# Performance work log

Measured on AMD Instinct MI355X. Metric: run time of the kernel, lower is better.

## Reference

```python
import jax, jax.numpy as jnp
import numpy as np

P = 12           # AR order == number of rollout steps
N = 2048         # input_size (nodes)
B = 128          # batch
C = 1            # channels (only channel 0 used)


def setup_inputs() -> dict:
    key = jax.random.key(0)
    kx, kw = jax.random.split(key)
    x = jax.random.normal(kx, (B, N, C, P), dtype=jnp.float32)
    W = jax.random.normal(kw, (P, N, N), dtype=jnp.float32)
    return {"x": x, "W": W}


def reference(x, W):
    # x: [B, N, C, L]; take channel 0 and transpose -> [B, L(=p), N]
    xt = jnp.transpose(x[:, :, 0, :], (0, 2, 1))

    def step(xc, _):
        # einsum('ijk,bik->bij') followed by sum over i fuses to 'ijk,bik->bj'
        y = jnp.einsum('ijk,bik->bj', W, xc)              # [B, N]
        xc = jnp.concatenate([xc[:, 1:, :], y[:, None, :]], axis=1)  # shift window
        return xc, y

    _, ys = jax.lax.scan(step, xt, None, length=12)       # ys: [12, B, N]
    return jnp.transpose(ys, (1, 2, 0))                   # [B, N, 12]
```

## Files before the change

### kernel.cpp

```cpp
#include <hip/hip_runtime.h>
#include <stdint.h>


typedef _Float16 f16x8 __attribute__((ext_vector_type(8)));
typedef float    f32x4 __attribute__((ext_vector_type(4)));

#define B_ 128
#define N_ 2048
#define P_ 12
#define K_ (P_*N_)
#define NT 16
#define NKP (K_/64)

#define WPK_BYTES    ((size_t)NT*NKP*16384)
#define H_SLOT_BYTES ((size_t)B_*N_*2)
#define H_BYTES      (23*H_SLOT_BYTES)
#define CH_BYTES     ((size_t)B_*N_*2)
#define PF_BYTES     (78*CH_BYTES)
#define PFB_BYTES    (44*CH_BYTES)
#define WS_NEEDED    (WPK_BYTES + H_BYTES + PF_BYTES + PFB_BYTES)

__device__ __constant__ int E_TAB[11] = {7, 13, 18, 24, 29, 35, 40, 46, 51, 57, 62};

__device__ __forceinline__ float pow2f(int e) {
    return __uint_as_float((uint32_t)(127 + e) << 23);
}

union F16x8 { _Float16 h[8]; uint4 q; };
union F16x4v { _Float16 h[4]; uint2 q; };

__device__ __forceinline__ uint32_t h_off(int slot, int b, int k) {
    uint32_t t = (uint32_t)((b << 6) + ((k & 31) << 1)) ^ (uint32_t)((b & 7) << 4);
    return (uint32_t)slot * (uint32_t)H_SLOT_BYTES + (uint32_t)(k >> 5) * 8192u + t;
}
__device__ __forceinline__ size_t w_tile_base(int nt, int pk) {
    return ((size_t)nt * NKP + (size_t)pk) * 16384;
}

__global__ void prep_all(const float* __restrict__ x, const float* __restrict__ W,
                         char* __restrict__ Wp, char* __restrict__ H)
{
    __shared__ float tile[128][68];
    int bid = blockIdx.x, t = threadIdx.x;
    if (bid < 128) {
        int tg = bid * 256 + t;
        int b = tg >> 8;
        int n0 = (tg & 255) << 3;
        const float4* s4 = (const float4*)(x + ((size_t)b * N_ + n0) * P_);
        float4 tmp[24];
        #pragma unroll
        for (int i2 = 0; i2 < 24; ++i2) tmp[i2] = s4[i2];
        #pragma unroll
        for (int p = 0; p < 12; ++p) {
            F16x8 o;
            #pragma unroll
            for (int q = 0; q < 8; ++q) {
                int fi = q * 12 + p;
                float4 blk = tmp[fi >> 2];
                float f = ((fi & 3) == 0) ? blk.x : ((fi & 3) == 1) ? blk.y : ((fi & 3) == 2) ? blk.z : blk.w;
                o.h[q] = (_Float16)f;
            }
            *(uint4*)(H + h_off(p, b, n0)) = o.q;
        }
        return;
    }
    int u = bid - 128;
    int nt = u / NKP, pk = u % NKP;
    int i  = pk >> 5;
    int k0 = (pk & 31) << 6;
    int j0 = nt << 7;
    #pragma unroll
    for (int pass = 0; pass < 8; ++pass) {
        int jl = pass * 16 + (t >> 4);
        int kq = (t & 15) * 4;
        float4 v = *(const float4*)(W + ((size_t)i * N_ + (j0 + jl)) * N_ + k0 + kq);
        tile[jl][kq + 0] = v.x; tile[jl][kq + 1] = v.y;
        tile[jl][kq + 2] = v.z; tile[jl][kq + 3] = v.w;
    }
    __syncthreads();
    int ksub = t >> 7, c = t & 127;
    char* base = Wp + w_tile_base(nt, pk) + (ksub << 13);
    #pragma unroll
    for (int ko = 0; ko < 4; ++ko) {
        F16x8 o;
        #pragma unroll
        for (int q = 0; q < 8; ++q) o.h[q] = (_Float16)tile[c][ksub * 32 + ko * 8 + q];
        uint32_t off = (uint32_t)((c << 6) + (ko << 4)) ^ (uint32_t)((c & 7) << 4);
        *(uint4*)(base + off) = o.q;
    }
}

__device__ __forceinline__ void gemm_body(
        const char* __restrict__ Wp, const char* __restrict__ H,
        _Float16* __restrict__ part, char* ldsAB,
        int nt, int pk0, int slot, int k0, int nph)
{
    const int tid  = threadIdx.x;
    const int lane = tid & 63;
    const int wv   = tid >> 6;
    const int wr   = wv >> 1;
    const int wc   = wv & 1;
    const int l15  = lane & 15;
    const int ko   = lane >> 4;
    const int jbase = (nt << 7) + (wc << 6) + l15;

    uint32_t aoff[4], boff[4];
    #pragma unroll
    for (int m = 0; m < 4; ++m) {
        int row = (wr << 6) + (m << 4) + l15;
        aoff[m] = (uint32_t)((row << 6) + (ko << 4)) ^ (uint32_t)((row & 7) << 4);
    }
    #pragma unroll
    for (int nf = 0; nf < 4; ++nf) {
        int c = (wc << 6) + (nf << 4) + l15;
        boff[nf] = (uint32_t)((c << 6) + (ko << 4)) ^ (uint32_t)((c & 7) << 4);
    }

    auto stage = [&](int buf, int ph) {
        int k = k0 + (ph << 5);
        const char* sA = H + (size_t)slot * H_SLOT_BYTES + (uint32_t)((k >> 5) << 13);
        const char* sB = Wp + w_tile_base(nt, pk0 + (ph >> 1)) + (uint32_t)((ph & 1) << 13);
        #pragma unroll
        for (int j = 0; j < 2; ++j) {
            uint32_t o = (uint32_t)(j << 12) + (uint32_t)(tid << 4);
            uint32_t d = (uint32_t)(j << 12) + (uint32_t)(wv << 10);
            __builtin_amdgcn_global_load_lds(
                (const __attribute__((address_space(1))) void*)(sA + o),
                (__attribute__((address_space(3))) void*)(ldsAB + buf * 16384 + d), 16, 0, 0);
            __builtin_amdgcn_global_load_lds(
                (const __attribute__((address_space(1))) void*)(sB + o),
                (__attribute__((address_space(3))) void*)(ldsAB + buf * 16384 + 8192 + d), 16, 0, 0);
        }
    };

    f32x4 acc[4][4];
    #pragma unroll
    for (int m = 0; m < 4; ++m)
        #pragma unroll
        for (int n = 0; n < 4; ++n) acc[m][n] = (f32x4){0.f, 0.f, 0.f, 0.f};

    stage(0, 0);
    stage(1, 1);
    asm volatile("s_waitcnt vmcnt(4) lgkmcnt(0)" ::: "memory");
    __builtin_amdgcn_s_barrier();

    int cur = 0;
    #pragma unroll 1
    for (int ph = 0; ph < nph; ++ph) {
        int nxt2 = cur + 2; if (nxt2 >= 3) nxt2 -= 3;
        if (ph + 2 < nph) stage(nxt2, ph + 2);
        const char* lA = ldsAB + cur * 16384;
        const char* lB = lA + 8192;
        f16x8 ah[4], bf[4];
        #pragma unroll
        for (int m = 0; m < 4; ++m) ah[m] = *(const f16x8*)(lA + aoff[m]);
        #pragma unroll
        for (int nf = 0; nf < 4; ++nf) bf[nf] = *(const f16x8*)(lB + boff[nf]);
        #pragma unroll
        for (int m = 0; m < 4; ++m)
            #pragma unroll
            for (int nf = 0; nf < 4; ++nf)
                acc[m][nf] = __builtin_amdgcn_mfma_f32_16x16x32_f16(ah[m], bf[nf], acc[m][nf], 0, 0, 0);
        if (ph + 1 < nph) {
            if (ph + 2 < nph) asm volatile("s_waitcnt vmcnt(4) lgkmcnt(0)" ::: "memory");
            else              asm volatile("s_waitcnt vmcnt(0) lgkmcnt(0)" ::: "memory");
            __builtin_amdgcn_s_barrier();
        }
        ++cur; if (cur == 3) cur = 0;
    }

    const int r0 = (lane >> 4) << 2;
    _Float16* pb = part + ((size_t)((wr << 6) + r0)) * N_ + jbase;
    #pragma unroll
    for (int m = 0; m < 4; ++m)
        #pragma unroll
        for (int n = 0; n < 4; ++n)
            #pragma unroll
            for (int r = 0; r < 4; ++r)
                pb[(size_t)(m * 16 + r) * N_ + n * 16] = (_Float16)acc[m][n][r];
}

__global__ __launch_bounds__(256, 3) void gemm_F(
        const char* __restrict__ Wp, const char* __restrict__ H,
        _Float16* __restrict__ pF)
{
    __shared__ alignas(16) char ldsAB[3 * 16384];
    int bid = blockIdx.x;
    int bucket = bid / 96;
    int w = bid % 96;
    int m  = w >> 3;
    int g  = bucket * 8 + (w & 7);
    int j  = g >> 4;
    int nt = g & 15;
    int s  = j + m;
    if (s > 11) return;
    int t = m;
    int idx = t * 12 - t * (t - 1) / 2 + j;
    gemm_body(Wp, H, pF + (size_t)idx * (CH_BYTES / 2), ldsAB,
              nt, j * 32, s, 0, 64);
}

__global__ __launch_bounds__(256, 3) void gemm_FB(
        const char* __restrict__ Wp, const char* __restrict__ H,
        _Float16* __restrict__ pFB, int t)
{
    __shared__ alignas(16) char ldsAB[3 * 16384];
    int c = blockIdx.x >> 4, nt = blockIdx.x & 15;
    int j = c >> 2, sub = c & 3;
    int i = 12 - t + j;
    gemm_body(Wp, H, pFB + (size_t)c * (CH_BYTES / 2), ldsAB,
              nt, i * 32 + sub * 8, 12 + j, sub * 512, 16);
}

__global__ void reduce_step(const _Float16* __restrict__ pF, const _Float16* __restrict__ pFB,
                            float* __restrict__ out, char* __restrict__ H, int t)
{
    int tid = blockIdx.x * 256 + threadIdx.x;
    int b = tid >> 9;
    int n0 = (tid & 511) << 2;
    const size_t eo = (size_t)b * N_ + n0;
    float s0 = 0.f, s1 = 0.f, s2 = 0.f, s3 = 0.f;
    int baseT = t * 12 - t * (t - 1) / 2;
    int nF = 12 - t;
    #pragma unroll 4
    for (int f = 0; f < nF; ++f) {
        F16x4v p;
        p.q = *(const uint2*)(pF + (size_t)(baseT + f) * (CH_BYTES / 2) + eo);
        s0 += (float)p.h[0]; s1 += (float)p.h[1];
        s2 += (float)p.h[2]; s3 += (float)p.h[3];
    }
    #pragma unroll 4
    for (int c = 0; c < 4 * t; ++c) {
        float sc = pow2f(E_TAB[c >> 2]);
        F16x4v p;
        p.q = *(const uint2*)(pFB + (size_t)c * (CH_BYTES / 2) + eo);
        s0 += (float)p.h[0] * sc; s1 += (float)p.h[1] * sc;
        s2 += (float)p.h[2] * sc; s3 += (float)p.h[3] * sc;
    }
    float* ob = out + eo * P_ + t;
    ob[0 * P_] = s0; ob[1 * P_] = s1; ob[2 * P_] = s2; ob[3 * P_] = s3;
    if (t < 11) {
        float ds = pow2f(-E_TAB[t]);
        F16x4v o;
        o.h[0] = (_Float16)(s0 * ds); o.h[1] = (_Float16)(s1 * ds);
        o.h[2] = (_Float16)(s2 * ds); o.h[3] = (_Float16)(s3 * ds);
        *(uint2*)(H + h_off(12 + t, b, n0)) = o.q;
    }
}

__global__ void naive_step(const float* __restrict__ x, const float* __restrict__ W,
                           float* __restrict__ out, int t)
{
    int tid = blockIdx.x * 256 + threadIdx.x;
    int b = tid >> 11;
    int j = tid & (N_ - 1);
    float acc = 0.f;
    for (int i = 0; i < 12; ++i) {
        int g = t + i;
        const float* src = (g < 12) ? (x   + (size_t)b * (N_ * 12) + g)
                                    : (out + (size_t)b * (N_ * 12) + (g - 12));
        const float* wr = W + ((size_t)i * N_ + j) * N_;
        for (int k = 0; k < N_; ++k)
            acc += wr[k] * src[(size_t)k * 12];
    }
    out[((size_t)b * N_ + j) * 12 + t] = acc;
}

extern "C" void kernel_launch(void* const* d_in, const int* in_sizes, int n_in,
                              void* d_out, int out_size, void* d_ws, size_t ws_size,
                              hipStream_t stream)
{
    const float* x = (const float*)d_in[0];
    const float* W = (const float*)d_in[1];
    float* out = (float*)d_out;

    if (ws_size < WS_NEEDED) {
        for (int t = 0; t < 12; ++t)
            naive_step<<<1024, 256, 0, stream>>>(x, W, out, t);
        return;
    }

    char* Wp = (char*)d_ws;
    char* H  = Wp + WPK_BYTES;
    _Float16* pF  = (_Float16*)(H + H_BYTES);
    _Float16* pFB = (_Float16*)(H + H_BYTES + PF_BYTES);

    prep_all<<<6272, 256, 0, stream>>>(x, W, Wp, H);
    gemm_F<<<2304, 256, 0, stream>>>(Wp, H, pF);
    reduce_step<<<256, 256, 0, stream>>>(pF, pFB, out, H, 0);
    for (int t = 1; t < 12; ++t) {
        gemm_FB<<<64 * t, 256, 0, stream>>>(Wp, H, pFB, t);
        reduce_step<<<256, 256, 0, stream>>>(pF, pFB, out, H, t);
    }
}
```

Before: 444.4 us.

## Share each W tile across two history slots in the forward GEMM

Replaces the gemm_F kernel with gemm_F2, in which each block loads one W k-tile into LDS and multiplies it against two adjacent history slots (s0 and s0+1), keeping two accumulator sets. This halves the W traffic per output chunk and cuts the grid from 2304 to 672 blocks. In exchange it doubles the accumulator registers, grows LDS per buffer to 24 KB, drops the launch-bounds occupancy hint from 3 to 2, and leaves some blocks with only one valid slot.

```diff
diff --git a/kernel.cpp b/kernel.cpp
--- a/kernel.cpp
+++ b/kernel.cpp
@@ -180,24 +180,132 @@
                 pb[(size_t)(m * 16 + r) * N_ + n * 16] = (_Float16)acc[m][n][r];
 }
 
-__global__ __launch_bounds__(256, 3) void gemm_F(
+__global__ __launch_bounds__(256, 2) void gemm_F2(
         const char* __restrict__ Wp, const char* __restrict__ H,
         _Float16* __restrict__ pF)
 {
-    __shared__ alignas(16) char ldsAB[3 * 16384];
-    int bid = blockIdx.x;
-    int bucket = bid / 96;
-    int w = bid % 96;
-    int m  = w >> 3;
-    int g  = bucket * 8 + (w & 7);
-    int j  = g >> 4;
-    int nt = g & 15;
-    int s  = j + m;
-    if (s > 11) return;
-    int t = m;
-    int idx = t * 12 - t * (t - 1) / 2 + j;
-    gemm_body(Wp, H, pF + (size_t)idx * (CH_BYTES / 2), ldsAB,
-              nt, j * 32, s, 0, 64);
+    __shared__ alignas(16) char ldsAB[3 * 24576];
+    const int tid  = threadIdx.x;
+    const int lane = tid & 63;
+    const int wv   = tid >> 6;
+    const int wr   = wv >> 1;
+    const int wc   = wv & 1;
+    const int l15  = lane & 15;
+    const int ko   = lane >> 4;
+    const int nt   = blockIdx.x & 15;
+    int pair = blockIdx.x >> 4;
+    int j = 0;
+    #pragma unroll 1
+    for (int jj = 0; jj < 12; ++jj) {
+        int cj = (12 - jj + 1) >> 1;
+        if (pair < cj) { j = jj; break; }
+        pair -= cj;
+    }
+    const int s0 = j + 2 * pair;
+    const int two = (s0 + 1 <= 11);
+    const int pk0 = j * 32;
+    const int jbase = (nt << 7) + (wc << 6) + l15;
+
+    uint32_t aoff[4], boff[4];
+    #pragma unroll
+    for (int m = 0; m < 4; ++m) {
+        int row = (wr << 6) + (m << 4) + l15;
+        aoff[m] = (uint32_t)((row << 6) + (ko << 4)) ^ (uint32_t)((row & 7) << 4);
+    }
+    #pragma unroll
+    for (int nf = 0; nf < 4; ++nf) {
+        int c = (wc << 6) + (nf << 4) + l15;
+        boff[nf] = (uint32_t)((c << 6) + (ko << 4)) ^ (uint32_t)((c & 7) << 4);
+    }
+
+    auto stage = [&](int buf, int ph) {
+        const uint32_t kb = (uint32_t)(ph << 13);
+        const char* sA0 = H + (size_t)s0 * H_SLOT_BYTES + kb;
+        const char* sA1 = H + (size_t)(s0 + (two ? 1 : 0)) * H_SLOT_BYTES + kb;
+        const char* sB  = Wp + w_tile_base(nt, pk0 + (ph >> 1)) + (uint32_t)((ph & 1) << 13);
+        #pragma unroll
+        for (int jj = 0; jj < 2; ++jj) {
+            uint32_t o = (uint32_t)(jj << 12) + (uint32_t)(tid << 4);
+            uint32_t d = (uint32_t)(jj << 12) + (uint32_t)(wv << 10);
+            char* db = ldsAB + buf * 24576 + d;
+            __builtin_amdgcn_global_load_lds(
+                (const __attribute__((address_space(1))) void*)(sA0 + o),
+                (__attribute__((address_space(3))) void*)(db), 16, 0, 0);
+            __builtin_amdgcn_global_load_lds(
+                (const __attribute__((address_space(1))) void*)(sA1 + o),
+                (__attribute__((address_space(3))) void*)(db + 8192), 16, 0, 0);
+            __builtin_amdgcn_global_load_lds(
+                (const __attribute__((address_space(1))) void*)(sB + o),
+                (__attribute__((address_space(3))) void*)(db + 16384), 16, 0, 0);
+        }
+    };
+
+    f32x4 acc[2][4][4];
+    #pragma unroll
+    for (int g = 0; g < 2; ++g)
+        #pragma unroll
+        for (int m = 0; m < 4; ++m)
+            #pragma unroll
+            for (int n = 0; n < 4; ++n) acc[g][m][n] = (f32x4){0.f, 0.f, 0.f, 0.f};
+
+    stage(0, 0);
+    stage(1, 1);
+    asm volatile("s_waitcnt vmcnt(6) lgkmcnt(0)" ::: "memory");
+    __builtin_amdgcn_s_barrier();
+
+    int cur = 0;
+    #pragma unroll 1
+    for (int ph = 0; ph < 64; ++ph) {
+        int nxt2 = cur + 2; if (nxt2 >= 3) nxt2 -= 3;
+        if (ph + 2 < 64) stage(nxt2, ph + 2);
+        const char* lb = ldsAB + cur * 24576;
+        f16x8 bf[4];
+        #pragma unroll
+        for (int nf = 0; nf < 4; ++nf) bf[nf] = *(const f16x8*)(lb + 16384 + boff[nf]);
+        {
+            f16x8 ah[4];
+            #pragma unroll
+            for (int m = 0; m < 4; ++m) ah[m] = *(const f16x8*)(lb + aoff[m]);
+            #pragma unroll
+            for (int m = 0; m < 4; ++m)
+                #pragma unroll
+                for (int nf = 0; nf < 4; ++nf)
+                    acc[0][m][nf] = __builtin_amdgcn_mfma_f32_16x16x32_f16(ah[m], bf[nf], acc[0][m][nf], 0, 0, 0);
+        }
+        if (two) {
+            f16x8 ah[4];
+            #pragma unroll
+            for (int m = 0; m < 4; ++m) ah[m] = *(const f16x8*)(lb + 8192 + aoff[m]);
+            #pragma unroll
+            for (int m = 0; m < 4; ++m)
+                #pragma unroll
+                for (int nf = 0; nf < 4; ++nf)
+                    acc[1][m][nf] = __builtin_amdgcn_mfma_f32_16x16x32_f16(ah[m], bf[nf], acc[1][m][nf], 0, 0, 0);
+        }
+        if (ph + 1 < 64) {
+            if (ph + 2 < 64) asm volatile("s_waitcnt vmcnt(6) lgkmcnt(0)" ::: "memory");
+            else             asm volatile("s_waitcnt vmcnt(0) lgkmcnt(0)" ::: "memory");
+            __builtin_amdgcn_s_barrier();
+        }
+        ++cur; if (cur == 3) cur = 0;
+    }
+
+    const int r0 = (lane >> 4) << 2;
+    #pragma unroll
+    for (int g = 0; g < 2; ++g) {
+        if (g == 1 && !two) break;
+        int t = s0 + g - j;
+        int idx = t * 12 - t * (t - 1) / 2 + j;
+        _Float16* pb = pF + (size_t)idx * (CH_BYTES / 2)
+                     + ((size_t)((wr << 6) + r0)) * N_ + jbase;
+        #pragma unroll
+        for (int m = 0; m < 4; ++m)
+            #pragma unroll
+            for (int n = 0; n < 4; ++n)
+                #pragma unroll
+                for (int r = 0; r < 4; ++r)
+                    pb[(size_t)(m * 16 + r) * N_ + n * 16] = (_Float16)acc[g][m][n][r];
+    }
 }
 
 __global__ __launch_bounds__(256, 3) void gemm_FB(
@@ -286,7 +394,7 @@
     _Float16* pFB = (_Float16*)(H + H_BYTES + PF_BYTES);
 
     prep_all<<<6272, 256, 0, stream>>>(x, W, Wp, H);
-    gemm_F<<<2304, 256, 0, stream>>>(Wp, H, pF);
+    gemm_F2<<<672, 256, 0, stream>>>(Wp, H, pF);
     reduce_step<<<256, 256, 0, stream>>>(pF, pFB, out, H, 0);
     for (int t = 1; t < 12; ++t) {
         gemm_FB<<<64 * t, 256, 0, stream>>>(Wp, H, pFB, t);
```

Result: no change. 443.7 us, median of 2 (-0.2%).

## Replace upfront full-history GEMM with per-step mixed GEMM of split-K chunks

Applied to the files above, without the earlier changes.

The single large upfront gemm_F launch, which computed every known-input contribution for all steps, is removed. Each step now launches one gemm_mix kernel that computes that step's known-input partial products, split into two K-halves, together with its feedback partials. This spreads the work evenly across steps and splits K for more parallelism, at the cost of twice as many fp16 partial buffers to write and reduce, plus a larger workspace.

```diff
diff --git a/kernel.cpp b/kernel.cpp
--- a/kernel.cpp
+++ b/kernel.cpp
@@ -16,7 +16,7 @@
 #define H_SLOT_BYTES ((size_t)B_*N_*2)
 #define H_BYTES      (23*H_SLOT_BYTES)
 #define CH_BYTES     ((size_t)B_*N_*2)
-#define PF_BYTES     (78*CH_BYTES)
+#define PF_BYTES     (156*CH_BYTES)
 #define PFB_BYTES    (44*CH_BYTES)
 #define WS_NEEDED    (WPK_BYTES + H_BYTES + PF_BYTES + PFB_BYTES)
 
@@ -180,36 +180,26 @@
                 pb[(size_t)(m * 16 + r) * N_ + n * 16] = (_Float16)acc[m][n][r];
 }
 
-__global__ __launch_bounds__(256, 3) void gemm_F(
+__global__ __launch_bounds__(256, 3) void gemm_mix(
         const char* __restrict__ Wp, const char* __restrict__ H,
-        _Float16* __restrict__ pF)
+        _Float16* __restrict__ pF, _Float16* __restrict__ pFB, int t)
 {
     __shared__ alignas(16) char ldsAB[3 * 16384];
-    int bid = blockIdx.x;
-    int bucket = bid / 96;
-    int w = bid % 96;
-    int m  = w >> 3;
-    int g  = bucket * 8 + (w & 7);
-    int j  = g >> 4;
-    int nt = g & 15;
-    int s  = j + m;
-    if (s > 11) return;
-    int t = m;
-    int idx = t * 12 - t * (t - 1) / 2 + j;
-    gemm_body(Wp, H, pF + (size_t)idx * (CH_BYTES / 2), ldsAB,
-              nt, j * 32, s, 0, 64);
-}
-
-__global__ __launch_bounds__(256, 3) void gemm_FB(
-        const char* __restrict__ Wp, const char* __restrict__ H,
-        _Float16* __restrict__ pFB, int t)
-{
-    __shared__ alignas(16) char ldsAB[3 * 16384];
-    int c = blockIdx.x >> 4, nt = blockIdx.x & 15;
-    int j = c >> 2, sub = c & 3;
-    int i = 12 - t + j;
-    gemm_body(Wp, H, pFB + (size_t)c * (CH_BYTES / 2), ldsAB,
-              nt, i * 32 + sub * 8, 12 + j, sub * 512, 16);
+    const int nt = blockIdx.x & 15;
+    const int c  = blockIdx.x >> 4;
+    const int nF2 = 2 * (12 - t);
+    if (c < nF2) {
+        int f = c >> 1, sub = c & 1;
+        int baseT = t * 12 - t * (t - 1) / 2;
+        gemm_body(Wp, H, pF + (size_t)((baseT + f) * 2 + sub) * (CH_BYTES / 2), ldsAB,
+                  nt, f * 32 + sub * 16, t + f, sub * 1024, 32);
+    } else {
+        int cf = c - nF2;
+        int jj = cf >> 2, sub = cf & 3;
+        int i = 12 - t + jj;
+        gemm_body(Wp, H, pFB + (size_t)cf * (CH_BYTES / 2), ldsAB,
+                  nt, i * 32 + sub * 8, 12 + jj, sub * 512, 16);
+    }
 }
 
 __global__ void reduce_step(const _Float16* __restrict__ pF, const _Float16* __restrict__ pFB,
@@ -220,12 +210,12 @@
     int n0 = (tid & 511) << 2;
     const size_t eo = (size_t)b * N_ + n0;
     float s0 = 0.f, s1 = 0.f, s2 = 0.f, s3 = 0.f;
-    int baseT = t * 12 - t * (t - 1) / 2;
-    int nF = 12 - t;
+    int base2 = (t * 12 - t * (t - 1) / 2) * 2;
+    int nF2 = 2 * (12 - t);
     #pragma unroll 4
-    for (int f = 0; f < nF; ++f) {
+    for (int f = 0; f < nF2; ++f) {
         F16x4v p;
-        p.q = *(const uint2*)(pF + (size_t)(baseT + f) * (CH_BYTES / 2) + eo);
+        p.q = *(const uint2*)(pF + (size_t)(base2 + f) * (CH_BYTES / 2) + eo);
         s0 += (float)p.h[0]; s1 += (float)p.h[1];
         s2 += (float)p.h[2]; s3 += (float)p.h[3];
     }
@@ -286,10 +276,9 @@
     _Float16* pFB = (_Float16*)(H + H_BYTES + PF_BYTES);
 
     prep_all<<<6272, 256, 0, stream>>>(x, W, Wp, H);
-    gemm_F<<<2304, 256, 0, stream>>>(Wp, H, pF);
-    reduce_step<<<256, 256, 0, stream>>>(pF, pFB, out, H, 0);
-    for (int t = 1; t < 12; ++t) {
-        gemm_FB<<<64 * t, 256, 0, stream>>>(Wp, H, pFB, t);
+    for (int t = 0; t < 12; ++t) {
+        int grid = (2 * (12 - t) + 4 * t) * 16;
+        gemm_mix<<<grid, 256, 0, stream>>>(Wp, H, pF, pFB, t);
         reduce_step<<<256, 256, 0, stream>>>(pF, pFB, out, H, t);
     }
 }
```

Measured after the change: 494.1 us. +11.2%, slower.
